# Kernel optimization log

Hardware: AMD Instinct MI355X
Metric: run time of the kernel (lower is better)

The kernel has to match this reference:

```python
import jax, jax.numpy as jnp
import numpy as np

D_MODEL = 512
N_QUBITS = 10
N_LAYERS = 2
N_TOKENS = 16384
DIM = 2 ** N_QUBITS


def _rx(t):
    c = jnp.cos(t / 2) + 0j
    s = -1j * jnp.sin(t / 2)
    return jnp.stack([jnp.stack([c, s]), jnp.stack([s, c])]).astype(jnp.complex64)


def _ry(t):
    c = jnp.cos(t / 2) + 0j
    s = jnp.sin(t / 2) + 0j
    return jnp.stack([jnp.stack([c, -s]), jnp.stack([s, c])]).astype(jnp.complex64)


def _rz(t):
    z = jnp.zeros((), jnp.complex64)
    return jnp.stack([jnp.stack([jnp.exp(-1j * t / 2), z]),
                      jnp.stack([z, jnp.exp(1j * t / 2)])]).astype(jnp.complex64)


def _apply_1q(state, q, U, n):
    # state: [B, 2^n]; qubit 0 is the most significant bit
    B = state.shape[0]
    s = state.reshape(B, 2 ** q, 2, 2 ** (n - q - 1))
    s = jnp.einsum('ij,bajk->baik', U, s)
    return s.reshape(B, 2 ** n)


def _simulate(psi, rot, ent, n):
    # psi: [B, 2^n] complex64. rot: [L, n, 3]. ent: [L, n-1].
    L = rot.shape[0]
    idx = jnp.arange(2 ** n)
    for l in range(L):
        for q in range(n):
            psi = _apply_1q(psi, q, _rx(rot[l, q, 0]), n)
            psi = _apply_1q(psi, q, _ry(rot[l, q, 1]), n)
            psi = _apply_1q(psi, q, _rz(rot[l, q, 2]), n)
        for i in range(n - 1):  # nearest-neighbor parameterized CZ (controlled-phase)
            q1, q2 = i, i + 1
            both = (((idx >> (n - 1 - q1)) & 1) & ((idx >> (n - 1 - q2)) & 1)) == 1
            phase = jnp.where(both, jnp.exp(1j * ent[l, i].astype(jnp.complex64)),
                              jnp.ones((), jnp.complex64))
            psi = psi * phase
    return psi


def setup_inputs() -> dict:
    key = jax.random.key(0)
    ks = jax.random.split(key, 6)
    return {
        'x': jax.random.normal(ks[0], (N_TOKENS, D_MODEL), jnp.float32),
        'W_in': jax.random.normal(ks[1], (DIM, D_MODEL), jnp.float32) / np.sqrt(D_MODEL),
        'b_in': jnp.zeros((DIM,), jnp.float32),
        'W_out': jax.random.normal(ks[2], (D_MODEL, DIM), jnp.float32) / np.sqrt(DIM),
        'b_out': jnp.zeros((D_MODEL,), jnp.float32),
        'rot': jax.random.normal(ks[3], (N_LAYERS, N_QUBITS, 3), jnp.float32),
        'ent': jax.random.normal(ks[4], (N_LAYERS, N_QUBITS - 1), jnp.float32),
        'ln_w': jnp.ones((D_MODEL,), jnp.float32),
        'ln_b': jnp.zeros((D_MODEL,), jnp.float32),
    }


def reference(x, W_in, b_in, W_out, b_out, rot, ent, ln_w, ln_b):
    n = rot.shape[1]
    # input projection to 2^n amplitudes, then L2-normalize (F.normalize, eps=1e-12)
    xq = x @ W_in.T + b_in
    norm = jnp.maximum(jnp.linalg.norm(xq, axis=-1, keepdims=True), 1e-12)
    psi = (xq / norm).astype(jnp.complex64)
    psi = _simulate(psi, rot, ent, n)
    probs = (psi.real ** 2 + psi.imag ** 2).astype(x.dtype)  # |amp|^2
    out = probs @ W_out.T + b_out
    # LayerNorm(d_model), eps=1e-5
    mu = jnp.mean(out, axis=-1, keepdims=True)
    var = jnp.mean((out - mu) ** 2, axis=-1, keepdims=True)
    return (out - mu) / jnp.sqrt(var + 1e-5) * ln_w + ln_b
```

## Files before the change

### kernel.cpp

```cpp
#include <hip/hip_runtime.h>
#include <cstdint>

#define TOKENS 16384
#define DMODEL 512
#define DIM    1024
#define NQ     10
#define NL     2
#define BM     128
#define BN     128
#define BK     32

typedef __bf16 bf16x8 __attribute__((ext_vector_type(8)));
typedef float  f32x4  __attribute__((ext_vector_type(4)));
typedef unsigned short u16x8 __attribute__((ext_vector_type(8)));

__device__ __forceinline__ float b2f(unsigned short h) {
    union { unsigned u; float f; } v; v.u = ((unsigned)h) << 16; return v.f;
}
__device__ __forceinline__ unsigned short f2b(float f) {
    unsigned u = __builtin_bit_cast(unsigned, f);
    return (unsigned short)((u + 0x7FFFu + ((u >> 16) & 1u)) >> 16);
}
__device__ __forceinline__ float2 cmul(float2 a, float2 b) {
    return make_float2(a.x * b.x - a.y * b.y, a.x * b.y + a.y * b.x);
}
__device__ __forceinline__ float2 cadd(float2 a, float2 b) {
    return make_float2(a.x + b.x, a.y + b.y);
}
__device__ __forceinline__ void async_copy16(const void* g, void* l) {
    __builtin_amdgcn_global_load_lds((const __attribute__((address_space(1))) void*)g,
                                     (__attribute__((address_space(3))) void*)l, 16, 0, 0);
}

__global__ __launch_bounds__(256)
void prep_all_kernel(const float* __restrict__ x,  unsigned short* __restrict__ xb,
                     const float* __restrict__ w2, unsigned short* __restrict__ w2b,
                     const float* __restrict__ W_in, unsigned short* __restrict__ wtT,
                     const float* __restrict__ rot, const float* __restrict__ ent,
                     const float* __restrict__ bin,
                     unsigned short* __restrict__ U, float* __restrict__ b2) {
    const int bid = blockIdx.x;
    const int t = threadIdx.x;

    if (bid < 256) {
        __shared__ float2 Gs[NL * NQ * 4];
        const int lane = t & 63;
        const int c = bid * 4 + (t >> 6);

        if (t < NL * NQ) {
            float tx = rot[t * 3 + 0] * 0.5f;
            float ty = rot[t * 3 + 1] * 0.5f;
            float tz = rot[t * 3 + 2] * 0.5f;
            float cx = cosf(tx), sx = sinf(tx);
            float cy = cosf(ty), sy = sinf(ty);
            float cz = cosf(tz), sz = sinf(tz);
            float2 rx00 = make_float2(cx, 0.f),  rx01 = make_float2(0.f, -sx);
            float2 rx10 = make_float2(0.f, -sx), rx11 = make_float2(cx, 0.f);
            float2 ry00 = make_float2(cy, 0.f),  ry01 = make_float2(-sy, 0.f);
            float2 ry10 = make_float2(sy, 0.f),  ry11 = make_float2(cy, 0.f);
            float2 m00 = cadd(cmul(ry00, rx00), cmul(ry01, rx10));
            float2 m01 = cadd(cmul(ry00, rx01), cmul(ry01, rx11));
            float2 m10 = cadd(cmul(ry10, rx00), cmul(ry11, rx10));
            float2 m11 = cadd(cmul(ry10, rx01), cmul(ry11, rx11));
            float2 e0 = make_float2(cz, -sz), e1 = make_float2(cz, sz);
            Gs[t * 4 + 0] = cmul(e0, m00);
            Gs[t * 4 + 1] = cmul(e0, m01);
            Gs[t * 4 + 2] = cmul(e1, m10);
            Gs[t * 4 + 3] = cmul(e1, m11);
        }
        float ef[NL * (NQ - 1)];
        #pragma unroll
        for (int i = 0; i < NL * (NQ - 1); i++) ef[i] = ent[i];
        __syncthreads();

        float2 amp[16];
        #pragma unroll
        for (int r = 0; r < 16; r++)
            amp[r] = make_float2((lane * 16 + r == c) ? 1.f : 0.f, 0.f);

        #pragma unroll 1
        for (int li = 0; li < NL; li++) {
            const int l = NL - 1 - li;
            #pragma unroll
            for (int r = 0; r < 16; r++) {
                int idx = lane * 16 + r;
                float ang = 0.f;
                #pragma unroll
                for (int q = 0; q < NQ - 1; q++) {
                    int both = ((idx >> (9 - q)) & 1) & ((idx >> (8 - q)) & 1);
                    if (both) ang += ef[l * (NQ - 1) + q];
                }
                amp[r] = cmul(amp[r], make_float2(cosf(ang), sinf(ang)));
            }
            const float2* Gl = Gs + l * NQ * 4;
            #pragma unroll
            for (int qq = 0; qq < NQ; qq++) {
                const int q = 9 - qq;
                float2 u00 = Gl[q * 4 + 0], u10 = Gl[q * 4 + 1];
                float2 u01 = Gl[q * 4 + 2], u11 = Gl[q * 4 + 3];
                if (q >= 6) {
                    const int S = 1 << (9 - q);
                    #pragma unroll
                    for (int r = 0; r < 16; r++) {
                        if (r & S) continue;
                        float2 a = amp[r], b = amp[r + S];
                        float2 n0, n1;
                        n0.x = u00.x * a.x - u00.y * a.y + u01.x * b.x - u01.y * b.y;
                        n0.y = u00.x * a.y + u00.y * a.x + u01.x * b.y + u01.y * b.x;
                        n1.x = u10.x * a.x - u10.y * a.y + u11.x * b.x - u11.y * b.y;
                        n1.y = u10.x * a.y + u10.y * a.x + u11.x * b.y + u11.y * b.x;
                        amp[r] = n0; amp[r + S] = n1;
                    }
                } else {
                    const int mask = 32 >> q;
                    int bit = (lane >> (5 - q)) & 1;
                    float2 ua = bit ? u11 : u00;
                    float2 ub = bit ? u10 : u01;
                    #pragma unroll
                    for (int r = 0; r < 16; r++) {
                        float px = __shfl_xor(amp[r].x, mask, 64);
                        float py = __shfl_xor(amp[r].y, mask, 64);
                        float nx = ua.x * amp[r].x - ua.y * amp[r].y + ub.x * px - ub.y * py;
                        float ny = ua.x * amp[r].y + ua.y * amp[r].x + ub.x * py + ub.y * px;
                        amp[r] = make_float2(nx, ny);
                    }
                }
            }
        }

        float accRe = 0.f, accIm = 0.f;
        #pragma unroll
        for (int i = 0; i < 4; i++) {
            float4 bv = *(const float4*)&bin[lane * 16 + i * 4];
            accRe += amp[i * 4 + 0].x * bv.x + amp[i * 4 + 1].x * bv.y
                   + amp[i * 4 + 2].x * bv.z + amp[i * 4 + 3].x * bv.w;
            accIm += amp[i * 4 + 0].y * bv.x + amp[i * 4 + 1].y * bv.y
                   + amp[i * 4 + 2].y * bv.z + amp[i * 4 + 3].y * bv.w;
        }
        #pragma unroll
        for (int m = 1; m < 64; m <<= 1) {
            accRe += __shfl_xor(accRe, m, 64);
            accIm += __shfl_xor(accIm, m, 64);
        }
        const int nR = ((c >> 4) << 5) + (c & 15);
        if (lane == 0) { b2[nR] = accRe; b2[nR + 16] = accIm; }

        u16x8 o0, o1, p0, p1;
        #pragma unroll
        for (int r = 0; r < 8; r++) {
            o0[r] = f2b(amp[r].x);     o1[r] = f2b(amp[r + 8].x);
            p0[r] = f2b(amp[r].y);     p1[r] = f2b(amp[r + 8].y);
        }
        unsigned short* rowRe = U + (size_t)nR * DIM + lane * 16;
        unsigned short* rowIm = U + (size_t)(nR + 16) * DIM + lane * 16;
        *(u16x8*)rowRe = o0; *(u16x8*)(rowRe + 8) = o1;
        *(u16x8*)rowIm = p0; *(u16x8*)(rowIm + 8) = p1;
        return;
    }

    if (bid < 768) {
        __shared__ float tile[32][33];
        const int b2i = bid - 256;
        const int tx = t & 31, ty = t >> 5;
        const int d0 = (b2i & 15) * 32, j0 = (b2i >> 4) * 32;
        #pragma unroll
        for (int i = 0; i < 32; i += 8)
            tile[ty + i][tx] = W_in[(size_t)(j0 + ty + i) * DMODEL + d0 + tx];
        __syncthreads();
        #pragma unroll
        for (int i = 0; i < 32; i += 8)
            wtT[(size_t)(d0 + ty + i) * DIM + j0 + tx] = f2b(tile[tx][ty + i]);
        return;
    }

    const int NX4 = TOKENS * DMODEL / 4;
    const int NW4 = DMODEL * DIM / 4;
    const int total = NX4 + NW4;
    const int stride = 2048 * 256;
    for (int i = (bid - 768) * 256 + t; i < total; i += stride) {
        const float* s; unsigned short* d; int j;
        if (i < NX4) { s = x;  d = xb;  j = i; }
        else         { s = w2; d = w2b; j = i - NX4; }
        float4 v = *(const float4*)&s[(size_t)j * 4];
        ushort4 o;
        o.x = f2b(v.x); o.y = f2b(v.y); o.z = f2b(v.z); o.w = f2b(v.w);
        *(ushort4*)&d[(size_t)j * 4] = o;
    }
}

__global__ __launch_bounds__(256)
void fold_kernel(const unsigned short* __restrict__ A, const unsigned short* __restrict__ B,
                 unsigned short* __restrict__ C) {
    __shared__ unsigned short sm[2 * 8192];
    const int t = threadIdx.x;
    const int wave = t >> 6, lane = t & 63;
    const int wm = wave >> 1, wn = wave & 1;
    const int laneR = lane & 15;
    const int bm0 = blockIdx.y * 64;
    const int bn0 = blockIdx.x * 64;

    const int csrc = (t & 7) ^ ((t >> 3) & 7);
    const int rowg = t >> 3;
    const unsigned aOff0 = (unsigned)(bm0 + rowg) * DIM + csrc * 8;
    const unsigned aOff1 = (unsigned)(bm0 + 32 + rowg) * DIM + csrc * 8;
    const unsigned bOff0 = (unsigned)(bn0 + rowg) * DIM + csrc * 8;
    const unsigned bOff1 = (unsigned)(bn0 + 32 + rowg) * DIM + csrc * 8;

    f32x4 acc[2][2] = {};

    #define F_STAGE(nbuf, kt) {                                            \
        unsigned short* d = sm + (nbuf) * 8192 + t * 8;                    \
        async_copy16(A + aOff0 + (kt) * 64, d);                            \
        async_copy16(A + aOff1 + (kt) * 64, d + 2048);                     \
        async_copy16(B + bOff0 + (kt) * 64, d + 4096);                     \
        async_copy16(B + bOff1 + (kt) * 64, d + 6144);                     \
    }

    F_STAGE(0, 0);
    asm volatile("s_waitcnt vmcnt(0)" ::: "memory");
    __syncthreads();

    #pragma unroll
    for (int kt = 0; kt < 16; kt++) {
        const int cur = kt & 1;
        if (kt < 15) F_STAGE(cur ^ 1, kt + 1);
        const unsigned short* la = sm + cur * 8192;
        const unsigned short* lb = la + 4096;
        #pragma unroll
        for (int kk = 0; kk < 2; kk++) {
            bf16x8 af[2], bfr[2];
            #pragma unroll
            for (int i = 0; i < 2; i++) {
                int row = wm * 32 + i * 16 + laneR;
                int slot = ((lane >> 4) + kk * 4) ^ (row & 7);
                af[i] = *(const bf16x8*)&la[row * 64 + slot * 8];
                int nrow = wn * 32 + i * 16 + laneR;
                int nslot = ((lane >> 4) + kk * 4) ^ (nrow & 7);
                bfr[i] = *(const bf16x8*)&lb[nrow * 64 + nslot * 8];
            }
            #pragma unroll
            for (int i = 0; i < 2; i++)
                #pragma unroll
                for (int j = 0; j < 2; j++)
                    acc[i][j] = __builtin_amdgcn_mfma_f32_16x16x32_bf16(af[i], bfr[j], acc[i][j], 0, 0, 0);
        }
        asm volatile("s_waitcnt vmcnt(0)" ::: "memory");
        __syncthreads();
    }
    #undef F_STAGE

    #pragma unroll
    for (int i = 0; i < 2; i++)
        #pragma unroll
        for (int j = 0; j < 2; j++) {
            int col = bn0 + wn * 32 + j * 16 + laneR;
            #pragma unroll
            for (int r = 0; r < 4; r++) {
                int row = bm0 + wm * 32 + i * 16 + (lane >> 4) * 4 + r;
                C[(size_t)row * DMODEL + col] = f2b(acc[i][j][r]);
            }
        }
}

__global__ __launch_bounds__(512, 2)
void gemm1_kernel(const unsigned short* __restrict__ A, const unsigned short* __restrict__ B,
                  const float* __restrict__ bias, unsigned short* __restrict__ P) {
    const int K = DMODEL;
    __shared__ unsigned short sm[2 * 32768];
    const int t = threadIdx.x;
    const int wave = t >> 6, lane = t & 63;
    const int wm = wave >> 2, wn = wave & 3;
    const int laneR = lane & 15;

    const int bid = blockIdx.x;
    const int swz = (bid & 7) * 64 + (bid >> 3);
    const int bm0 = (swz >> 3) * 256;
    const int bn0 = (swz & 7) * 256;

    const int csrc = (t & 3) ^ ((t >> 3) & 3);
    const int rowg = t >> 2;
    const unsigned aOff0 = (unsigned)(bm0 + rowg) * DMODEL + csrc * 8;
    const unsigned aOff1 = (unsigned)(bm0 + 128 + rowg) * DMODEL + csrc * 8;
    const unsigned bOff0 = (unsigned)(bn0 + rowg) * DMODEL + csrc * 8;
    const unsigned bOff1 = (unsigned)(bn0 + 128 + rowg) * DMODEL + csrc * 8;

    const int slotc = (((lane >> 4) ^ ((lane >> 1) & 3)) & 3) * 8;

    f32x4 acc[8][4] = {};

    #define G1_STAGE(nbuf, kk, kb)                                                 \
    {                                                                              \
        unsigned short* d0 = sm + (nbuf) * 32768 + (kk) * 8192 + wave * 512;       \
        async_copy16(A + aOff0 + (kb) + (kk) * 32, d0);                            \
        async_copy16(A + aOff1 + (kb) + (kk) * 32, d0 + 4096);                     \
        async_copy16(B + bOff0 + (kb) + (kk) * 32, d0 + 16384);                    \
        async_copy16(B + bOff1 + (kb) + (kk) * 32, d0 + 20480);                    \
    }

    #define G1_COMPUTE(cbuf, kk)                                                   \
    {                                                                              \
        const unsigned short* la = sm + (cbuf) * 32768 + (kk) * 8192;              \
        const unsigned short* lb = la + 16384;                                     \
        bf16x8 af[8], bfr[4];                                                      \
        _Pragma("unroll")                                                          \
        for (int i = 0; i < 8; i++)                                                \
            af[i] = *(const bf16x8*)&la[(wm * 128 + i * 16 + laneR) * 32 + slotc]; \
        _Pragma("unroll")                                                          \
        for (int j = 0; j < 4; j++)                                                \
            bfr[j] = *(const bf16x8*)&lb[(wn * 64 + j * 16 + laneR) * 32 + slotc]; \
        __builtin_amdgcn_s_setprio(1);                                             \
        _Pragma("unroll")                                                          \
        for (int i = 0; i < 8; i++)                                                \
            _Pragma("unroll")                                                      \
            for (int j = 0; j < 4; j++)                                            \
                acc[i][j] = __builtin_amdgcn_mfma_f32_16x16x32_bf16(af[i], bfr[j], acc[i][j], 0, 0, 0); \
        __builtin_amdgcn_s_setprio(0);                                             \
    }

    G1_STAGE(0, 0, 0);
    G1_STAGE(0, 1, 0);
    asm volatile("s_waitcnt vmcnt(4)" ::: "memory");
    asm volatile("s_barrier" ::: "memory");

    #pragma unroll
    for (int kt = 0; kt < 7; kt++) {
        const int cur = kt & 1, nxt = cur ^ 1;
        const unsigned kb = (unsigned)(kt + 1) * 64;
        G1_STAGE(nxt, 0, kb);
        G1_COMPUTE(cur, 0);
        asm volatile("s_waitcnt vmcnt(4)" ::: "memory");
        asm volatile("s_barrier" ::: "memory");
        G1_STAGE(nxt, 1, kb);
        G1_COMPUTE(cur, 1);
        asm volatile("s_waitcnt vmcnt(4)" ::: "memory");
        asm volatile("s_barrier" ::: "memory");
    }
    G1_COMPUTE(1, 0);
    asm volatile("s_waitcnt vmcnt(0)" ::: "memory");
    asm volatile("s_barrier" ::: "memory");
    G1_COMPUTE(1, 1);

    #undef G1_STAGE
    #undef G1_COMPUTE

    #pragma unroll
    for (int i = 0; i < 8; i++) {
        #pragma unroll
        for (int jp = 0; jp < 2; jp++) {
            int colRe = bn0 + wn * 64 + jp * 32 + laneR;
            float bRe = bias[colRe];
            float bIm = bias[colRe + 16];
            int pc = (bn0 >> 1) + wn * 32 + jp * 16 + laneR;
            #pragma unroll
            for (int r = 0; r < 4; r++) {
                int row = bm0 + wm * 128 + i * 16 + (lane >> 4) * 4 + r;
                float vr = acc[i][2 * jp][r] + bRe;
                float vi = acc[i][2 * jp + 1][r] + bIm;
                P[(size_t)row * DIM + pc] = f2b(vr * vr + vi * vi);
            }
        }
    }
}

__global__ __launch_bounds__(512)
void gemm2_ln_kernel(const unsigned short* __restrict__ A,
                     const unsigned short* __restrict__ B,
                     const float* __restrict__ bias,
                     const float* __restrict__ lw, const float* __restrict__ lb,
                     float* __restrict__ out) {
    __shared__ unsigned short sm[2 * 36864];
    __shared__ float redS[4][64], redQ[4][64];
    __shared__ float muS[64], rsS[64], n2s[64];
    const int t = threadIdx.x, wave = t >> 6, lane = t & 63;
    const int wm = wave >> 2, wn = wave & 3;
    const int laneR = lane & 15;
    const int bm0 = blockIdx.x * 64;

    const int csrc = (t & 3) ^ ((t >> 3) & 3);
    const int akk  = t >> 8, arow = (t >> 2) & 63;
    const unsigned aSrc = (unsigned)(bm0 + arow) * DIM + akk * 32 + csrc * 8;
    const int brow = t >> 2;
    const int slotc = (((lane >> 4) ^ ((lane >> 1) & 3)) & 3) * 8;

    f32x4 acc[2][8] = {};
    f32x4 accN[2] = {};
    bf16x8 ones;
    #pragma unroll
    for (int r = 0; r < 8; r++) ones[r] = (__bf16)1.0f;

    #define G2_STAGE_A(nbuf, kb) {                                          \
        async_copy16(A + aSrc + (kb), sm + (nbuf) * 36864 + t * 8);         \
    }
    #define G2_STAGE_B(nbuf, kk, kb) {                                      \
        unsigned short* d = sm + (nbuf) * 36864 + 4096 + (kk) * 16384 + t * 8; \
        const unsigned short* s0 = B + (size_t)brow * DIM + (kb) + (kk) * 32 + csrc * 8; \
        async_copy16(s0,                 d);                                 \
        async_copy16(s0 + 128 * DIM,     d + 4096);                         \
        async_copy16(s0 + 256 * DIM,     d + 8192);                         \
        async_copy16(s0 + 384 * DIM,     d + 12288);                        \
    }
    #define G2_COMPUTE(cbuf, kk) {                                          \
        const unsigned short* la  = sm + (cbuf) * 36864 + (kk) * 2048;      \
        const unsigned short* lbp = sm + (cbuf) * 36864 + 4096 + (kk) * 16384; \
        bf16x8 af[2], bfr[8];                                               \
        _Pragma("unroll")                                                   \
        for (int i = 0; i < 2; i++)                                         \
            af[i] = *(const bf16x8*)&la[(wm * 32 + i * 16 + laneR) * 32 + slotc]; \
        _Pragma("unroll")                                                   \
        for (int j = 0; j < 8; j++)                                         \
            bfr[j] = *(const bf16x8*)&lbp[(wn * 128 + j * 16 + laneR) * 32 + slotc]; \
        __builtin_amdgcn_s_setprio(1);                                      \
        _Pragma("unroll")                                                   \
        for (int i = 0; i < 2; i++)                                         \
            _Pragma("unroll")                                               \
            for (int j = 0; j < 8; j++)                                     \
                acc[i][j] = __builtin_amdgcn_mfma_f32_16x16x32_bf16(af[i], bfr[j], acc[i][j], 0, 0, 0); \
        if (wn == 0) {                                                      \
            _Pragma("unroll")                                               \
            for (int i = 0; i < 2; i++)                                     \
                accN[i] = __builtin_amdgcn_mfma_f32_16x16x32_bf16(af[i], ones, accN[i], 0, 0, 0); \
        }                                                                   \
        __builtin_amdgcn_s_setprio(0);                                      \
    }

    G2_STAGE_A(0, 0); G2_STAGE_B(0, 0, 0); G2_STAGE_B(0, 1, 0);
    asm volatile("s_waitcnt vmcnt(4)" ::: "memory");
    asm volatile("s_barrier" ::: "memory");

    #pragma unroll
    for (int n = 0; n < 15; n++) {
        const int cb = n & 1, nb = cb ^ 1;
        const unsigned kb = (unsigned)(n + 1) * 64;
        G2_STAGE_A(nb, kb); G2_STAGE_B(nb, 0, kb);
        G2_COMPUTE(cb, 0);
        asm volatile("s_waitcnt vmcnt(5)" ::: "memory");
        asm volatile("s_barrier" ::: "memory");
        G2_STAGE_B(nb, 1, kb);
        G2_COMPUTE(cb, 1);
        asm volatile("s_waitcnt vmcnt(4)" ::: "memory");
        asm volatile("s_barrier" ::: "memory");
    }
    G2_COMPUTE(1, 0);
    asm volatile("s_waitcnt vmcnt(0)" ::: "memory");
    asm volatile("s_barrier" ::: "memory");
    G2_COMPUTE(1, 1);

    #undef G2_STAGE_A
    #undef G2_STAGE_B
    #undef G2_COMPUTE

    if (wn == 0 && laneR == 0) {
        #pragma unroll
        for (int i = 0; i < 2; i++)
            #pragma unroll
            for (int r = 0; r < 4; r++)
                n2s[wm * 32 + i * 16 + (lane >> 4) * 4 + r] = accN[i][r];
    }
    __syncthreads();

    float bvj[8];
    #pragma unroll
    for (int j = 0; j < 8; j++) bvj[j] = bias[wn * 128 + j * 16 + laneR];

    #pragma unroll
    for (int i = 0; i < 2; i++)
        #pragma unroll
        for (int r = 0; r < 4; r++) {
            int rl = wm * 32 + i * 16 + (lane >> 4) * 4 + r;
            float nn = 1.0f / fmaxf(n2s[rl], 1e-24f);
            float s = 0.f, q = 0.f;
            #pragma unroll
            for (int j = 0; j < 8; j++) {
                float val = acc[i][j][r] * nn + bvj[j];
                acc[i][j][r] = val;
                s += val; q += val * val;
            }
            s += __shfl_xor(s, 1, 64); q += __shfl_xor(q, 1, 64);
            s += __shfl_xor(s, 2, 64); q += __shfl_xor(q, 2, 64);
            s += __shfl_xor(s, 4, 64); q += __shfl_xor(q, 4, 64);
            s += __shfl_xor(s, 8, 64); q += __shfl_xor(q, 8, 64);
            if (laneR == 0) { redS[wn][rl] = s; redQ[wn][rl] = q; }
        }
    __syncthreads();
    if (t < 64) {
        float s = redS[0][t] + redS[1][t] + redS[2][t] + redS[3][t];
        float q = redQ[0][t] + redQ[1][t] + redQ[2][t] + redQ[3][t];
        float mu = s * (1.0f / DMODEL);
        float var = q * (1.0f / DMODEL) - mu * mu;
        muS[t] = mu;
        rsS[t] = rsqrtf(var + 1e-5f);
    }
    __syncthreads();
    #pragma unroll
    for (int i = 0; i < 2; i++)
        #pragma unroll
        for (int j = 0; j < 8; j++) {
            int col = wn * 128 + j * 16 + laneR;
            float w = lw[col], bb = lb[col];
            #pragma unroll
            for (int r = 0; r < 4; r++) {
                int rl = wm * 32 + i * 16 + (lane >> 4) * 4 + r;
                out[(size_t)(bm0 + rl) * DMODEL + col] =
                    (acc[i][j][r] - muS[rl]) * rsS[rl] * w + bb;
            }
        }
}

extern "C" void kernel_launch(void* const* d_in, const int* in_sizes, int n_in,
                              void* d_out, int out_size, void* d_ws, size_t ws_size,
                              hipStream_t stream) {
    (void)in_sizes; (void)n_in; (void)out_size; (void)ws_size;
    const float* x     = (const float*)d_in[0];
    const float* W_in  = (const float*)d_in[1];
    const float* b_in  = (const float*)d_in[2];
    const float* W_out = (const float*)d_in[3];
    const float* b_out = (const float*)d_in[4];
    const float* rot   = (const float*)d_in[5];
    const float* ent   = (const float*)d_in[6];
    const float* ln_w  = (const float*)d_in[7];
    const float* ln_b  = (const float*)d_in[8];
    float* out = (float*)d_out;

    char* ws = (char*)d_ws;
    unsigned short* p    = (unsigned short*)ws;
    unsigned short* x_bf = (unsigned short*)(ws + 33554432ull);
    unsigned short* wtT  = (unsigned short*)(ws + 50331648ull);
    unsigned short* w2b  = (unsigned short*)(ws + 51380224ull);
    unsigned short* Ucat = (unsigned short*)(ws + 52428800ull);
    unsigned short* W1c  = (unsigned short*)(ws + 56623104ull);
    float*          b2   = (float*)(ws + 58720256ull);

    prep_all_kernel<<<2816, 256, 0, stream>>>(x, x_bf, W_out, w2b, W_in, wtT,
                                              rot, ent, b_in, Ucat, b2);
    fold_kernel<<<dim3(DMODEL / 64, 2 * DIM / 64), 256, 0, stream>>>(Ucat, wtT, W1c);
    gemm1_kernel<<<512, 512, 0, stream>>>(x_bf, W1c, b2, p);
    gemm2_ln_kernel<<<TOKENS / 64, 512, 0, stream>>>(
        p, w2b, b_out, ln_w, ln_b, out);
}
```

Before: 195.9 us.

## Interleave Re/Im columns for packed stores and spread norm MFMAs across waves

Reorders the combined unitary's rows so each lane's real/imag accumulator pairs map to adjacent probability columns. The GEMM1 epilogue can then write two bf16 probabilities per packed store and load its bias values once instead of per tile. In GEMM2, the extra row-norm MFMA work, which only wave column 0 used to do, now rotates across the four wave columns by k-step. The partial norms are then summed through shared memory, which costs an extra barrier. This aims to reduce store instruction count and balance MFMA load across waves.

New measurement: 196.7 us. No clear change (+0.4%).

```diff
diff --git a/kernel.cpp b/kernel.cpp
--- a/kernel.cpp
+++ b/kernel.cpp
@@ -142,7 +142,7 @@
             accRe += __shfl_xor(accRe, m, 64);
             accIm += __shfl_xor(accIm, m, 64);
         }
-        const int nR = ((c >> 4) << 5) + (c & 15);
+        const int nR = ((c >> 5) << 6) + ((c & 1) << 5) + ((c >> 1) & 15);
         if (lane == 0) { b2[nR] = accRe; b2[nR + 16] = accIm; }
 
         u16x8 o0, o1, p0, p1;
@@ -343,21 +343,23 @@
     #undef G1_STAGE
     #undef G1_COMPUTE
 
+    const int cb0 = bn0 + wn * 64 + laneR;
+    const float b0 = bias[cb0];
+    const float b1 = bias[cb0 + 16];
+    const float b2v = bias[cb0 + 32];
+    const float b3 = bias[cb0 + 48];
+    const int pc2 = (bn0 >> 1) + wn * 32 + laneR * 2;
     #pragma unroll
     for (int i = 0; i < 8; i++) {
         #pragma unroll
-        for (int jp = 0; jp < 2; jp++) {
-            int colRe = bn0 + wn * 64 + jp * 32 + laneR;
-            float bRe = bias[colRe];
-            float bIm = bias[colRe + 16];
-            int pc = (bn0 >> 1) + wn * 32 + jp * 16 + laneR;
-            #pragma unroll
-            for (int r = 0; r < 4; r++) {
-                int row = bm0 + wm * 128 + i * 16 + (lane >> 4) * 4 + r;
-                float vr = acc[i][2 * jp][r] + bRe;
-                float vi = acc[i][2 * jp + 1][r] + bIm;
-                P[(size_t)row * DIM + pc] = f2b(vr * vr + vi * vi);
-            }
+        for (int r = 0; r < 4; r++) {
+            int row = bm0 + wm * 128 + i * 16 + (lane >> 4) * 4 + r;
+            float v0 = acc[i][0][r] + b0, v1 = acc[i][1][r] + b1;
+            float v2 = acc[i][2][r] + b2v, v3 = acc[i][3][r] + b3;
+            ushort2 o;
+            o.x = f2b(v0 * v0 + v1 * v1);
+            o.y = f2b(v2 * v2 + v3 * v3);
+            *(ushort2*)&P[(size_t)row * DIM + pc2] = o;
         }
     }
 }
@@ -370,7 +372,7 @@
                      float* __restrict__ out) {
     __shared__ unsigned short sm[2 * 36864];
     __shared__ float redS[4][64], redQ[4][64];
-    __shared__ float muS[64], rsS[64], n2s[64];
+    __shared__ float muS[64], rsS[64], n2s[64], n2p[4][64];
     const int t = threadIdx.x, wave = t >> 6, lane = t & 63;
     const int wm = wave >> 2, wn = wave & 3;
     const int laneR = lane & 15;
@@ -399,7 +401,7 @@
         async_copy16(s0 + 256 * DIM,     d + 8192);                         \
         async_copy16(s0 + 384 * DIM,     d + 12288);                        \
     }
-    #define G2_COMPUTE(cbuf, kk) {                                          \
+    #define G2_COMPUTE(cbuf, kk, sel) {                                     \
         const unsigned short* la  = sm + (cbuf) * 36864 + (kk) * 2048;      \
         const unsigned short* lbp = sm + (cbuf) * 36864 + 4096 + (kk) * 16384; \
         bf16x8 af[2], bfr[8];                                               \
@@ -415,7 +417,7 @@
             _Pragma("unroll")                                               \
             for (int j = 0; j < 8; j++)                                     \
                 acc[i][j] = __builtin_amdgcn_mfma_f32_16x16x32_bf16(af[i], bfr[j], acc[i][j], 0, 0, 0); \
-        if (wn == 0) {                                                      \
+        if (wn == (sel)) {                                                  \
             _Pragma("unroll")                                               \
             for (int i = 0; i < 2; i++)                                     \
                 accN[i] = __builtin_amdgcn_mfma_f32_16x16x32_bf16(af[i], ones, accN[i], 0, 0, 0); \
@@ -432,30 +434,33 @@
         const int cb = n & 1, nb = cb ^ 1;
         const unsigned kb = (unsigned)(n + 1) * 64;
         G2_STAGE_A(nb, kb); G2_STAGE_B(nb, 0, kb);
-        G2_COMPUTE(cb, 0);
+        G2_COMPUTE(cb, 0, n & 3);
         asm volatile("s_waitcnt vmcnt(5)" ::: "memory");
         asm volatile("s_barrier" ::: "memory");
         G2_STAGE_B(nb, 1, kb);
-        G2_COMPUTE(cb, 1);
+        G2_COMPUTE(cb, 1, n & 3);
         asm volatile("s_waitcnt vmcnt(4)" ::: "memory");
         asm volatile("s_barrier" ::: "memory");
     }
-    G2_COMPUTE(1, 0);
+    G2_COMPUTE(1, 0, 3);
     asm volatile("s_waitcnt vmcnt(0)" ::: "memory");
     asm volatile("s_barrier" ::: "memory");
-    G2_COMPUTE(1, 1);
+    G2_COMPUTE(1, 1, 3);
 
     #undef G2_STAGE_A
     #undef G2_STAGE_B
     #undef G2_COMPUTE
 
-    if (wn == 0 && laneR == 0) {
+    if (laneR == 0) {
         #pragma unroll
         for (int i = 0; i < 2; i++)
             #pragma unroll
             for (int r = 0; r < 4; r++)
-                n2s[wm * 32 + i * 16 + (lane >> 4) * 4 + r] = accN[i][r];
-    }
+                n2p[wn][wm * 32 + i * 16 + (lane >> 4) * 4 + r] = accN[i][r];
+    }
+    __syncthreads();
+    if (t < 64)
+        n2s[t] = n2p[0][t] + n2p[1][t] + n2p[2][t] + n2p[3][t];
     __syncthreads();
 
     float bvj[8];
```
